# Optimization experiments

Measured on AMD Instinct MI355X. Metric: run time of the kernel, lower is better.

Reference implementation:

```python
import jax, jax.numpy as jnp
import numpy as np

B, F, N = 128, 256, 2000

def setup_inputs() -> dict:
    key = jax.random.key(0)
    ks = jax.random.split(key, 10)
    s = 0.05
    return {
        'nfeature': jax.random.normal(ks[0], (B, F, N, 1), jnp.float32),
        'last_current': jax.random.randint(ks[1], (B, 2), 0, N, jnp.int32),
        'Wg': jax.random.normal(ks[2], (F, F), jnp.float32) * s,
        'bg': jax.random.normal(ks[3], (F,), jnp.float32) * s,
        'Wnode': jax.random.normal(ks[4], (3 * F, F), jnp.float32) * s,
        'bnode': jax.random.normal(ks[5], (3 * F,), jnp.float32) * s,
        'Wlc': jax.random.normal(ks[6], (F, 2 * F), jnp.float32) * s,
        'blc': jax.random.normal(ks[7], (F,), jnp.float32) * s,
        'Wproj': jax.random.normal(ks[8], (F, F), jnp.float32) * s,
        'bproj': jax.random.normal(ks[9], (F,), jnp.float32) * s,
    }

def reference(nfeature, last_current, Wg, bg, Wnode, bnode, Wlc, blc, Wproj, bproj):
    # nfeature: [B, F, N, 1]
    x = nfeature[..., 0]                                  # [B, F, N]
    f = x.shape[1]
    scale = 1.0 / jnp.sqrt(jnp.asarray(f, x.dtype))
    # global fixed query: max over nodes then Linear
    glb = jnp.max(x, axis=2)                              # [B, F]
    Q = glb @ Wg.T + bg                                   # [B, F]
    # node embeddings via 1x1 conv == channel GEMM, split into K, V, logit_K
    kvl = jnp.einsum('bfn,gf->bgn', x, Wnode) + bnode[None, :, None]  # [B, 3F, N]
    K, V, Klog = jnp.split(kvl, 3, axis=1)                # each [B, F, N]
    # gather last/current city features
    lc = jnp.take_along_axis(x, last_current[:, None, :], axis=2)     # [B, F, 2]
    context = jnp.concatenate([lc[:, :, 0], lc[:, :, 1]], axis=1)     # [B, 2F]
    cQ = context @ Wlc.T + blc + Q                        # [B, F]
    # attention: single query over N keys
    ucj = jnp.einsum('bf,bfn->bn', cQ, K) * scale         # [B, N]
    attn = jax.nn.softmax(ucj, axis=1)
    nc = jnp.einsum('bn,bfn->bf', attn, V)                # [B, F]
    nc = nc @ Wproj.T + bproj                             # [B, F]
    logits = jnp.einsum('bf,bfn->bn', nc, Klog) * scale   # [B, N]
    return jnp.tanh(logits) * 10.0
```

## Files before the change

kernel.cpp:

```cpp
#include <hip/hip_runtime.h>
#include <hip/hip_fp16.h>
#include <math.h>

#define BB 128
#define FF 256
#define NN 2000
#define SW 8
#define SC 256

typedef float f32x4 __attribute__((ext_vector_type(4)));
union H8 { f32x4 v; __half2 h[4]; };

__device__ __forceinline__ float sel8(f32x4 a, f32x4 b, int e) {
    float v;
    switch (e) {
        case 0: v = a.x; break; case 1: v = a.y; break;
        case 2: v = a.z; break; case 3: v = a.w; break;
        case 4: v = b.x; break; case 5: v = b.y; break;
        case 6: v = b.z; break; default: v = b.w; break;
    }
    return v;
}

__global__ __launch_bounds__(256) void k_convmax(const float* __restrict__ x,
                                                 const int* __restrict__ lc,
                                                 __half* __restrict__ xh,
                                                 float* __restrict__ glb,
                                                 float* __restrict__ xg) {
    int row  = (blockIdx.x << 2) | (threadIdx.x >> 6);
    int lane = threadIdx.x & 63;
    int b    = row >> 8;
    const int c0 = lc[2 * b], c1 = lc[2 * b + 1];
    const int i0 = c0 >> 3, e0 = c0 & 7;
    const int i1 = c1 >> 3, e1 = c1 & 7;
    const f32x4* src = (const f32x4*)(x + (size_t)row * NN);
    f32x4*       dst = (f32x4*)(xh + (size_t)row * NN);
    float m = -INFINITY;
    for (int i = lane; i < 250; i += 64) {
        f32x4 a = __builtin_nontemporal_load(src + 2 * i);
        f32x4 q = __builtin_nontemporal_load(src + 2 * i + 1);
        m = fmaxf(m, fmaxf(fmaxf(a.x, a.y), fmaxf(a.z, a.w)));
        m = fmaxf(m, fmaxf(fmaxf(q.x, q.y), fmaxf(q.z, q.w)));
        if (i == i0) xg[row * 2]     = sel8(a, q, e0);
        if (i == i1) xg[row * 2 + 1] = sel8(a, q, e1);
        H8 o;
        o.h[0] = __floats2half2_rn(a.x, a.y);
        o.h[1] = __floats2half2_rn(a.z, a.w);
        o.h[2] = __floats2half2_rn(q.x, q.y);
        o.h[3] = __floats2half2_rn(q.z, q.w);
        dst[i] = o.v;
    }
#pragma unroll
    for (int off = 32; off; off >>= 1) m = fmaxf(m, __shfl_xor(m, off));
    if (!lane) glb[row] = m;
}

__global__ __launch_bounds__(256) void k_prep(
    const float* __restrict__ xg, const float* __restrict__ glb,
    const float* __restrict__ Wg, const float* __restrict__ bg,
    const float* __restrict__ Wnode, const float* __restrict__ bnode,
    const float* __restrict__ Wlc, const float* __restrict__ blc,
    float* __restrict__ cK, float* __restrict__ cK0)
{
    int b = blockIdx.x;
    int f = threadIdx.x;
    __shared__ float s_glb[FF], s_ctx[2 * FF], s_cQ[FF], s_red[FF];
    s_glb[f] = glb[b * FF + f];
    float2 g2 = ((const float2*)xg)[b * FF + f];
    s_ctx[f]      = g2.x;
    s_ctx[FF + f] = g2.y;
    __syncthreads();
    const float* wg = Wg + (size_t)f * FF;
    float q0 = 0, q1 = 0, q2 = 0, q3 = 0;
    for (int j = 0; j < FF; j += 4) {
        q0 = fmaf(wg[j],     s_glb[j],     q0);
        q1 = fmaf(wg[j + 1], s_glb[j + 1], q1);
        q2 = fmaf(wg[j + 2], s_glb[j + 2], q2);
        q3 = fmaf(wg[j + 3], s_glb[j + 3], q3);
    }
    const float* wl = Wlc + (size_t)f * 2 * FF;
    for (int j = 0; j < 2 * FF; j += 4) {
        q0 = fmaf(wl[j],     s_ctx[j],     q0);
        q1 = fmaf(wl[j + 1], s_ctx[j + 1], q1);
        q2 = fmaf(wl[j + 2], s_ctx[j + 2], q2);
        q3 = fmaf(wl[j + 3], s_ctx[j + 3], q3);
    }
    float cq = bg[f] + blc[f] + ((q0 + q1) + (q2 + q3));
    s_cQ[f]  = cq;
    s_red[f] = cq * bnode[f];
    __syncthreads();
    float c0 = 0, c1 = 0;
    for (int g = 0; g < FF; g += 2) {
        c0 = fmaf(s_cQ[g],     Wnode[(size_t)g * FF + f],       c0);
        c1 = fmaf(s_cQ[g + 1], Wnode[(size_t)(g + 1) * FF + f], c1);
    }
    cK[b * FF + f] = c0 + c1;
    for (int s = 128; s > 0; s >>= 1) {
        if (f < s) s_red[f] += s_red[f + s];
        __syncthreads();
    }
    if (f == 0) cK0[b] = s_red[0];
}

__global__ __launch_bounds__(512) void k_attn(
    const __half* __restrict__ xh,
    const float* __restrict__ cK, const float* __restrict__ cK0,
    float* __restrict__ y_part, float* __restrict__ m_part,
    float* __restrict__ s_part)
{
    int b = blockIdx.x >> 3, st = blockIdx.x & 7;
    int tid = threadIdx.x, w = tid >> 6, lane = tid & 63;
    int par = lane >> 5, chunk = lane & 31;
    __shared__ __half tile[FF][SC];
    __shared__ float s_u[8][SC];
    __shared__ float s_p[SC];
    __shared__ float s_cK[FF];
    __shared__ float s_red[8], s_red2[8];
    if (tid < FF) s_cK[tid] = cK[b * FF + tid];
    __syncthreads();

    int colbase = (st << 8) + (chunk << 3);
    bool cvalid = colbase < NN;
    const __half* base = xh + ((size_t)(b * FF) + (w << 5) + par) * NN + colbase;

    float up0 = 0, up1 = 0, up2 = 0, up3 = 0, up4 = 0, up5 = 0, up6 = 0, up7 = 0;
#pragma unroll
    for (int g = 0; g < 4; ++g) {
        f32x4 hv[4];
#pragma unroll
        for (int r = 0; r < 4; ++r) {
            if (cvalid) hv[r] = *(const f32x4*)(base + (size_t)((g << 3) + (r << 1)) * NN);
            else        hv[r] = (f32x4){0.f, 0.f, 0.f, 0.f};
        }
#pragma unroll
        for (int r = 0; r < 4; ++r) {
            int row = (w << 5) + par + (g << 3) + (r << 1);
            *(f32x4*)&tile[row][(chunk ^ (row & 7)) << 3] = hv[r];
            H8 u; u.v = hv[r];
            float c = s_cK[row];
            float2 q0 = __half22float2(u.h[0]);
            float2 q1 = __half22float2(u.h[1]);
            float2 q2 = __half22float2(u.h[2]);
            float2 q3 = __half22float2(u.h[3]);
            up0 = fmaf(c, q0.x, up0); up1 = fmaf(c, q0.y, up1);
            up2 = fmaf(c, q1.x, up2); up3 = fmaf(c, q1.y, up3);
            up4 = fmaf(c, q2.x, up4); up5 = fmaf(c, q2.y, up5);
            up6 = fmaf(c, q3.x, up6); up7 = fmaf(c, q3.y, up7);
        }
    }
    up0 += __shfl_xor(up0, 32); up1 += __shfl_xor(up1, 32);
    up2 += __shfl_xor(up2, 32); up3 += __shfl_xor(up3, 32);
    up4 += __shfl_xor(up4, 32); up5 += __shfl_xor(up5, 32);
    up6 += __shfl_xor(up6, 32); up7 += __shfl_xor(up7, 32);
    if (!par) {
        f32x4 v0 = {up0, up1, up2, up3}, v1 = {up4, up5, up6, up7};
        *(f32x4*)&s_u[w][chunk << 3]       = v0;
        *(f32x4*)&s_u[w][(chunk << 3) + 4] = v1;
    }
    __syncthreads();

    const float scale = 0.0625f;
    float uu = -INFINITY;
    if (tid < SC) {
        int col = (st << 8) + tid;
        if (col < NN) {
            float usum = 0.f;
#pragma unroll
            for (int ww = 0; ww < 8; ++ww) usum += s_u[ww][tid];
            uu = (usum + cK0[b]) * scale;
        }
    }
    float m = uu;
#pragma unroll
    for (int off = 32; off; off >>= 1) m = fmaxf(m, __shfl_xor(m, off));
    if (!lane && w < 4) s_red[w] = m;
    __syncthreads();
    float M = fmaxf(fmaxf(s_red[0], s_red[1]), fmaxf(s_red[2], s_red[3]));
    float e = (uu > -INFINITY) ? __expf(uu - M) : 0.f;
    if (tid < SC) s_p[tid] = e;
    float ssum = e;
#pragma unroll
    for (int off = 32; off; off >>= 1) ssum += __shfl_xor(ssum, off);
    if (!lane && w < 4) s_red2[w] = ssum;
    __syncthreads();
    if (!tid) {
        m_part[(b << 3) + st] = M;
        s_part[(b << 3) + st] = s_red2[0] + s_red2[1] + s_red2[2] + s_red2[3];
    }

    f32x4 pv0 = *(const f32x4*)&s_p[chunk << 3];
    f32x4 pv1 = *(const f32x4*)&s_p[(chunk << 3) + 4];
    float acc[16];
#pragma unroll
    for (int k = 0; k < 16; ++k) {
        int row = (w << 5) + par + (k << 1);
        H8 u; u.v = *(const f32x4*)&tile[row][(chunk ^ (row & 7)) << 3];
        float2 q0 = __half22float2(u.h[0]);
        float2 q1 = __half22float2(u.h[1]);
        float2 q2 = __half22float2(u.h[2]);
        float2 q3 = __half22float2(u.h[3]);
        float a = 0.f;
        a = fmaf(pv0.x, q0.x, a); a = fmaf(pv0.y, q0.y, a);
        a = fmaf(pv0.z, q1.x, a); a = fmaf(pv0.w, q1.y, a);
        a = fmaf(pv1.x, q2.x, a); a = fmaf(pv1.y, q2.y, a);
        a = fmaf(pv1.z, q3.x, a); a = fmaf(pv1.w, q3.y, a);
        acc[k] = a;
    }
    __syncthreads();
    float* tbuf = (float*)&tile[0][0];
#pragma unroll
    for (int k = 0; k < 16; ++k)
        tbuf[(w << 10) + ((par + (k << 1)) << 5) + chunk] = acc[k];
    __syncthreads();
    {
        int row = tid >> 1, half = tid & 1;
        const float* src = tbuf + ((row >> 5) << 10) + ((row & 31) << 5) + (half << 4);
        f32x4 a0 = *(const f32x4*)src;
        f32x4 a1 = *(const f32x4*)(src + 4);
        f32x4 a2 = *(const f32x4*)(src + 8);
        f32x4 a3 = *(const f32x4*)(src + 12);
        float sm = ((a0.x + a0.y) + (a0.z + a0.w)) + ((a1.x + a1.y) + (a1.z + a1.w)) +
                   ((a2.x + a2.y) + (a2.z + a2.w)) + ((a3.x + a3.y) + (a3.z + a3.w));
        sm += __shfl_xor(sm, 1);
        if (!half) y_part[(size_t)((b << 3) + st) * FF + row] = sm;
    }
}

__global__ __launch_bounds__(256) void k_dense(
    const float* __restrict__ y_part, const float* __restrict__ m_part,
    const float* __restrict__ s_part,
    const float* __restrict__ Wnode, const float* __restrict__ bnode,
    const float* __restrict__ Wproj, const float* __restrict__ bproj,
    float* __restrict__ cL, float* __restrict__ cL0)
{
    int b = blockIdx.x;
    int f = threadIdx.x;
    int wid = f >> 6, lane = f & 63;
    __shared__ float s_y[FF], s_v[FF], s_red[4];

    float M = -INFINITY;
#pragma unroll
    for (int s = 0; s < 8; ++s) M = fmaxf(M, m_part[(b << 3) + s]);
    float S = 0.f, wgt[8];
#pragma unroll
    for (int s = 0; s < 8; ++s) {
        wgt[s] = __expf(m_part[(b << 3) + s] - M);
        S = fmaf(wgt[s], s_part[(b << 3) + s], S);
    }
    float invS = 1.0f / S;
    float acc = 0.f;
#pragma unroll
    for (int s = 0; s < 8; ++s)
        acc = fmaf(wgt[s], y_part[(size_t)((b << 3) + s) * FF + f], acc);
    s_y[f] = acc * invS;
    __syncthreads();

    const float* wv = Wnode + (size_t)(FF + f) * FF;
    float a0 = 0, a1 = 0, a2 = 0, a3 = 0;
    for (int j = 0; j < FF; j += 4) {
        a0 = fmaf(wv[j],     s_y[j],     a0);
        a1 = fmaf(wv[j + 1], s_y[j + 1], a1);
        a2 = fmaf(wv[j + 2], s_y[j + 2], a2);
        a3 = fmaf(wv[j + 3], s_y[j + 3], a3);
    }
    s_v[f] = bnode[FF + f] + ((a0 + a1) + (a2 + a3));
    __syncthreads();
    const float* wp = Wproj + (size_t)f * FF;
    a0 = 0; a1 = 0; a2 = 0; a3 = 0;
    for (int j = 0; j < FF; j += 4) {
        a0 = fmaf(wp[j],     s_v[j],     a0);
        a1 = fmaf(wp[j + 1], s_v[j + 1], a1);
        a2 = fmaf(wp[j + 2], s_v[j + 2], a2);
        a3 = fmaf(wp[j + 3], s_v[j + 3], a3);
    }
    float nc2 = bproj[f] + ((a0 + a1) + (a2 + a3));
    __syncthreads();
    s_v[f] = nc2;
    __syncthreads();
    float c0 = 0, c1 = 0;
    for (int g = 0; g < FF; g += 2) {
        c0 = fmaf(s_v[g],     Wnode[(size_t)(2 * FF + g) * FF + f],     c0);
        c1 = fmaf(s_v[g + 1], Wnode[(size_t)(2 * FF + g + 1) * FF + f], c1);
    }
    cL[b * FF + f] = c0 + c1;
    float t = nc2 * bnode[2 * FF + f];
#pragma unroll
    for (int off = 32; off; off >>= 1) t += __shfl_xor(t, off);
    if (!lane) s_red[wid] = t;
    __syncthreads();
    if (!f) cL0[b] = s_red[0] + s_red[1] + s_red[2] + s_red[3];
}

__global__ __launch_bounds__(512) void k_logits(const __half* __restrict__ xh,
                                                const float* __restrict__ cL,
                                                const float* __restrict__ cL0,
                                                float* __restrict__ out)
{
    int b = blockIdx.x >> 3, st = blockIdx.x & 7;
    int tid = threadIdx.x, w = tid >> 6, lane = tid & 63;
    int par = lane >> 5, chunk = lane & 31;
    __shared__ float s_cL[FF];
    __shared__ float s_acc[8][SC];
    if (tid < FF) s_cL[tid] = cL[b * FF + tid];
    __syncthreads();

    int colbase = (st << 8) + (chunk << 3);
    bool cvalid = colbase < NN;
    const __half* base = xh + ((size_t)(b * FF) + (w << 5) + par) * NN + colbase;
    float up0 = 0, up1 = 0, up2 = 0, up3 = 0, up4 = 0, up5 = 0, up6 = 0, up7 = 0;
    if (cvalid) {
#pragma unroll
        for (int g = 0; g < 4; ++g) {
            f32x4 hv[4];
#pragma unroll
            for (int r = 0; r < 4; ++r)
                hv[r] = *(const f32x4*)(base + (size_t)((g << 3) + (r << 1)) * NN);
#pragma unroll
            for (int r = 0; r < 4; ++r) {
                int row = (w << 5) + par + (g << 3) + (r << 1);
                H8 u; u.v = hv[r];
                float c = s_cL[row];
                float2 q0 = __half22float2(u.h[0]);
                float2 q1 = __half22float2(u.h[1]);
                float2 q2 = __half22float2(u.h[2]);
                float2 q3 = __half22float2(u.h[3]);
                up0 = fmaf(c, q0.x, up0); up1 = fmaf(c, q0.y, up1);
                up2 = fmaf(c, q1.x, up2); up3 = fmaf(c, q1.y, up3);
                up4 = fmaf(c, q2.x, up4); up5 = fmaf(c, q2.y, up5);
                up6 = fmaf(c, q3.x, up6); up7 = fmaf(c, q3.y, up7);
            }
        }
    }
    up0 += __shfl_xor(up0, 32); up1 += __shfl_xor(up1, 32);
    up2 += __shfl_xor(up2, 32); up3 += __shfl_xor(up3, 32);
    up4 += __shfl_xor(up4, 32); up5 += __shfl_xor(up5, 32);
    up6 += __shfl_xor(up6, 32); up7 += __shfl_xor(up7, 32);
    if (!par) {
        f32x4 v0 = {up0, up1, up2, up3}, v1 = {up4, up5, up6, up7};
        *(f32x4*)&s_acc[w][chunk << 3]       = v0;
        *(f32x4*)&s_acc[w][(chunk << 3) + 4] = v1;
    }
    __syncthreads();
    if (tid < SC) {
        int col = (st << 8) + tid;
        if (col < NN) {
            float t = 0.f;
#pragma unroll
            for (int ww = 0; ww < 8; ++ww) t += s_acc[ww][tid];
            out[(size_t)b * NN + col] = tanhf((t + cL0[b]) * 0.0625f) * 10.f;
        }
    }
}

extern "C" void kernel_launch(void* const* d_in, const int* in_sizes, int n_in,
                              void* d_out, int out_size, void* d_ws, size_t ws_size,
                              hipStream_t stream) {
    const float* x     = (const float*)d_in[0];
    const int*   lc    = (const int*)d_in[1];
    const float* Wg    = (const float*)d_in[2];
    const float* bg    = (const float*)d_in[3];
    const float* Wnode = (const float*)d_in[4];
    const float* bnode = (const float*)d_in[5];
    const float* Wlc   = (const float*)d_in[6];
    const float* blc   = (const float*)d_in[7];
    const float* Wproj = (const float*)d_in[8];
    const float* bproj = (const float*)d_in[9];
    float* out = (float*)d_out;

    float* ws     = (float*)d_ws;
    float* glb    = ws + 0;
    float* xg     = ws + 32768;
    float* cK     = ws + 98304;
    float* cK0    = ws + 131072;
    float* m_part = ws + 132096;
    float* s_part = ws + 134144;
    float* cL     = ws + 136192;
    float* cL0    = ws + 168960;
    float* y_part = ws + 169984;
    __half* xh    = (__half*)(ws + (2 << 20));

    k_convmax<<<BB * FF / 4, 256, 0, stream>>>(x, lc, xh, glb, xg);
    k_prep   <<<BB, 256, 0, stream>>>(xg, glb, Wg, bg, Wnode, bnode, Wlc, blc, cK, cK0);
    k_attn   <<<BB * SW, 512, 0, stream>>>(xh, cK, cK0, y_part, m_part, s_part);
    k_dense  <<<BB, 256, 0, stream>>>(y_part, m_part, s_part, Wnode, bnode, Wproj, bproj, cL, cL0);
    k_logits <<<BB * SW, 512, 0, stream>>>(xh, cL, cL0, out);
}
```

Baseline: 193.8 us.

## Drop LDS half tile in attention kernel; re-read x from global and batch more loads

The attention kernel no longer stages the 256x256 half-precision tile of x in shared memory. It re-reads the same slice from global memory (expected to hit L2) for the weighted V sum, which shrinks LDS use and should allow more resident blocks. Loads in both the attention and logits kernels are batched 8 at a time instead of 4, giving more memory-level parallelism at the cost of extra registers. The risk is the duplicated global traffic in the attention kernel if the second read misses cache.

```diff
diff --git a/kernel.cpp b/kernel.cpp
--- a/kernel.cpp
+++ b/kernel.cpp
@@ -111,7 +111,7 @@
     int b = blockIdx.x >> 3, st = blockIdx.x & 7;
     int tid = threadIdx.x, w = tid >> 6, lane = tid & 63;
     int par = lane >> 5, chunk = lane & 31;
-    __shared__ __half tile[FF][SC];
+    __shared__ float tbuf[8][1024];
     __shared__ float s_u[8][SC];
     __shared__ float s_p[SC];
     __shared__ float s_cK[FF];
@@ -122,20 +122,18 @@
     int colbase = (st << 8) + (chunk << 3);
     bool cvalid = colbase < NN;
     const __half* base = xh + ((size_t)(b * FF) + (w << 5) + par) * NN + colbase;
+    const f32x4 zero = {0.f, 0.f, 0.f, 0.f};
 
     float up0 = 0, up1 = 0, up2 = 0, up3 = 0, up4 = 0, up5 = 0, up6 = 0, up7 = 0;
 #pragma unroll
-    for (int g = 0; g < 4; ++g) {
-        f32x4 hv[4];
-#pragma unroll
-        for (int r = 0; r < 4; ++r) {
-            if (cvalid) hv[r] = *(const f32x4*)(base + (size_t)((g << 3) + (r << 1)) * NN);
-            else        hv[r] = (f32x4){0.f, 0.f, 0.f, 0.f};
-        }
-#pragma unroll
-        for (int r = 0; r < 4; ++r) {
-            int row = (w << 5) + par + (g << 3) + (r << 1);
-            *(f32x4*)&tile[row][(chunk ^ (row & 7)) << 3] = hv[r];
+    for (int h = 0; h < 2; ++h) {
+        f32x4 hv[8];
+#pragma unroll
+        for (int r = 0; r < 8; ++r)
+            hv[r] = cvalid ? *(const f32x4*)(base + (size_t)((h << 4) + (r << 1)) * NN) : zero;
+#pragma unroll
+        for (int r = 0; r < 8; ++r) {
+            int row = (w << 5) + par + (h << 4) + (r << 1);
             H8 u; u.v = hv[r];
             float c = s_cK[row];
             float2 q0 = __half22float2(u.h[0]);
@@ -192,33 +190,38 @@
     f32x4 pv1 = *(const f32x4*)&s_p[(chunk << 3) + 4];
     float acc[16];
 #pragma unroll
-    for (int k = 0; k < 16; ++k) {
-        int row = (w << 5) + par + (k << 1);
-        H8 u; u.v = *(const f32x4*)&tile[row][(chunk ^ (row & 7)) << 3];
-        float2 q0 = __half22float2(u.h[0]);
-        float2 q1 = __half22float2(u.h[1]);
-        float2 q2 = __half22float2(u.h[2]);
-        float2 q3 = __half22float2(u.h[3]);
-        float a = 0.f;
-        a = fmaf(pv0.x, q0.x, a); a = fmaf(pv0.y, q0.y, a);
-        a = fmaf(pv0.z, q1.x, a); a = fmaf(pv0.w, q1.y, a);
-        a = fmaf(pv1.x, q2.x, a); a = fmaf(pv1.y, q2.y, a);
-        a = fmaf(pv1.z, q3.x, a); a = fmaf(pv1.w, q3.y, a);
-        acc[k] = a;
-    }
-    __syncthreads();
-    float* tbuf = (float*)&tile[0][0];
+    for (int h = 0; h < 2; ++h) {
+        f32x4 hv[8];
+#pragma unroll
+        for (int r = 0; r < 8; ++r)
+            hv[r] = cvalid ? *(const f32x4*)(base + (size_t)((h << 4) + (r << 1)) * NN) : zero;
+#pragma unroll
+        for (int r = 0; r < 8; ++r) {
+            H8 u; u.v = hv[r];
+            float2 q0 = __half22float2(u.h[0]);
+            float2 q1 = __half22float2(u.h[1]);
+            float2 q2 = __half22float2(u.h[2]);
+            float2 q3 = __half22float2(u.h[3]);
+            float a = 0.f;
+            a = fmaf(pv0.x, q0.x, a); a = fmaf(pv0.y, q0.y, a);
+            a = fmaf(pv0.z, q1.x, a); a = fmaf(pv0.w, q1.y, a);
+            a = fmaf(pv1.x, q2.x, a); a = fmaf(pv1.y, q2.y, a);
+            a = fmaf(pv1.z, q3.x, a); a = fmaf(pv1.w, q3.y, a);
+            acc[(h << 3) + r] = a;
+        }
+    }
+    __syncthreads();
 #pragma unroll
     for (int k = 0; k < 16; ++k)
-        tbuf[(w << 10) + ((par + (k << 1)) << 5) + chunk] = acc[k];
+        tbuf[w][((par + (k << 1)) << 5) + chunk] = acc[k];
     __syncthreads();
     {
         int row = tid >> 1, half = tid & 1;
-        const float* src = tbuf + ((row >> 5) << 10) + ((row & 31) << 5) + (half << 4);
-        f32x4 a0 = *(const f32x4*)src;
-        f32x4 a1 = *(const f32x4*)(src + 4);
-        f32x4 a2 = *(const f32x4*)(src + 8);
-        f32x4 a3 = *(const f32x4*)(src + 12);
+        const float* srcp = &tbuf[row >> 5][((row & 31) << 5) + (half << 4)];
+        f32x4 a0 = *(const f32x4*)srcp;
+        f32x4 a1 = *(const f32x4*)(srcp + 4);
+        f32x4 a2 = *(const f32x4*)(srcp + 8);
+        f32x4 a3 = *(const f32x4*)(srcp + 12);
         float sm = ((a0.x + a0.y) + (a0.z + a0.w)) + ((a1.x + a1.y) + (a1.z + a1.w)) +
                    ((a2.x + a2.y) + (a2.z + a2.w)) + ((a3.x + a3.y) + (a3.z + a3.w));
         sm += __shfl_xor(sm, 1);
@@ -307,28 +310,27 @@
     int colbase = (st << 8) + (chunk << 3);
     bool cvalid = colbase < NN;
     const __half* base = xh + ((size_t)(b * FF) + (w << 5) + par) * NN + colbase;
+    const f32x4 zero = {0.f, 0.f, 0.f, 0.f};
     float up0 = 0, up1 = 0, up2 = 0, up3 = 0, up4 = 0, up5 = 0, up6 = 0, up7 = 0;
-    if (cvalid) {
-#pragma unroll
-        for (int g = 0; g < 4; ++g) {
-            f32x4 hv[4];
-#pragma unroll
-            for (int r = 0; r < 4; ++r)
-                hv[r] = *(const f32x4*)(base + (size_t)((g << 3) + (r << 1)) * NN);
-#pragma unroll
-            for (int r = 0; r < 4; ++r) {
-                int row = (w << 5) + par + (g << 3) + (r << 1);
-                H8 u; u.v = hv[r];
-                float c = s_cL[row];
-                float2 q0 = __half22float2(u.h[0]);
-                float2 q1 = __half22float2(u.h[1]);
-                float2 q2 = __half22float2(u.h[2]);
-                float2 q3 = __half22float2(u.h[3]);
-                up0 = fmaf(c, q0.x, up0); up1 = fmaf(c, q0.y, up1);
-                up2 = fmaf(c, q1.x, up2); up3 = fmaf(c, q1.y, up3);
-                up4 = fmaf(c, q2.x, up4); up5 = fmaf(c, q2.y, up5);
-                up6 = fmaf(c, q3.x, up6); up7 = fmaf(c, q3.y, up7);
-            }
+#pragma unroll
+    for (int h = 0; h < 2; ++h) {
+        f32x4 hv[8];
+#pragma unroll
+        for (int r = 0; r < 8; ++r)
+            hv[r] = cvalid ? *(const f32x4*)(base + (size_t)((h << 4) + (r << 1)) * NN) : zero;
+#pragma unroll
+        for (int r = 0; r < 8; ++r) {
+            int row = (w << 5) + par + (h << 4) + (r << 1);
+            H8 u; u.v = hv[r];
+            float c = s_cL[row];
+            float2 q0 = __half22float2(u.h[0]);
+            float2 q1 = __half22float2(u.h[1]);
+            float2 q2 = __half22float2(u.h[2]);
+            float2 q3 = __half22float2(u.h[3]);
+            up0 = fmaf(c, q0.x, up0); up1 = fmaf(c, q0.y, up1);
+            up2 = fmaf(c, q1.x, up2); up3 = fmaf(c, q1.y, up3);
+            up4 = fmaf(c, q2.x, up4); up5 = fmaf(c, q2.y, up5);
+            up6 = fmaf(c, q3.x, up6); up7 = fmaf(c, q3.y, up7);
         }
     }
     up0 += __shfl_xor(up0, 32); up1 += __shfl_xor(up1, 32);
```

Measured after the change: 203.0 us. 1.05x slower.
